# Performance work log

Measured on AMD Instinct MI355X. Metric: run time of the kernel, lower is better.

Reference implementation:

```python
import jax, jax.numpy as jnp
import numpy as np

PI = 3.14159265358979323846
MARGIN = 6.0
DIM = 256
ENT_TOT = 43234
REL_RANGE = (6.0 + 2.0) / DIM  # (margin + epsilon) / dim = 0.03125


def setup_inputs() -> dict:
    key = jax.random.key(0)
    k1, k2, k3 = jax.random.split(key, 3)
    head = jax.random.normal(k1, (32, 2 * DIM), dtype=jnp.float32)
    relation = jax.random.normal(k2, (32, DIM), dtype=jnp.float32)
    ent_emb = jax.random.normal(k3, (ENT_TOT, 2 * DIM), dtype=jnp.float32)
    return {"head": head, "relation": relation, "ent_emb": ent_emb}


def reference(head, relation, ent_emb):
    # head: (B, 2D) -> re/im halves (B, D)
    re_h, im_h = jnp.split(head, 2, axis=-1)
    # entity table: (E, 2D) -> (E, D) each
    re_t, im_t = jnp.split(ent_emb, 2, axis=-1)
    # phase rotation from relation embedding
    phase = relation / (REL_RANGE / PI)          # (B, D)
    re_r = jnp.cos(phase)
    im_r = jnp.sin(phase)
    # complex rotation of head by relation: (B, D)
    re_rot = re_h * re_r - im_h * im_r
    im_rot = re_h * im_r + im_h * re_r
    # difference against every entity, broadcast to (B, E, D)
    re_s = re_rot[:, None, :] - re_t[None, :, :]
    im_s = im_rot[:, None, :] - im_t[None, :, :]
    # L2 norm over the complex pair, summed over D -> (B, E)
    dist = jnp.sqrt(re_s * re_s + im_s * im_s).sum(axis=-1)
    return MARGIN - dist
```

## Files before the change

### kernel.cpp

```cpp
#include <hip/hip_runtime.h>
#include <math.h>

#define DIMH 256
#define NB   32
#define E_TOT 43234
#define TE   32
#define DK   64
#define PHASE_SCALE 100.53096491487338

__global__ void rot_kernel(const float* __restrict__ head,
                           const float* __restrict__ rel,
                           float* __restrict__ rot) {
    int b = blockIdx.x;
    int d = threadIdx.x;
    float re_h = head[b * 2 * DIMH + d];
    float im_h = head[b * 2 * DIMH + DIMH + d];
    float ph_f = rel[b * DIMH + d] * (float)PHASE_SCALE;
    double s, c;
    sincos((double)ph_f, &s, &c);
    float re_r = (float)c, im_r = (float)s;
    rot[b * DIMH + d]             = re_h * re_r - im_h * im_r;
    rot[NB * DIMH + b * DIMH + d] = re_h * im_r + im_h * re_r;
}

__device__ __forceinline__ float cplx_abs(float a, float b) {
    return __builtin_amdgcn_sqrtf(fmaf(a, a, b * b));
}

__global__ __launch_bounds__(256) void dist_kernel(const float* __restrict__ ent,
                                                   const float* __restrict__ rot,
                                                   float* __restrict__ out) {
    __shared__ float s_er[TE][DK + 2];
    __shared__ float s_ei[TE][DK + 2];
    __shared__ float s_rr[NB][DK + 2];
    __shared__ float s_ri[NB][DK + 2];

    const int tid = threadIdx.x;
    const int eb  = blockIdx.x * TE;
    const int e0  = (tid & 15) * 2;
    const int b0  = (tid >> 4) * 2;

    float acc00 = 0.f, acc01 = 0.f, acc10 = 0.f, acc11 = 0.f;

    for (int dk = 0; dk < DIMH; dk += DK) {
        #pragma unroll
        for (int qq = 0; qq < 2; ++qq) {
            int q   = tid + qq * 256;
            int row = q >> 4;
            int col = (q & 15) << 2;
            int er  = min(eb + row, E_TOT - 1);
            float4 vre = *reinterpret_cast<const float4*>(&ent[(size_t)er * (2 * DIMH) + dk + col]);
            float4 vim = *reinterpret_cast<const float4*>(&ent[(size_t)er * (2 * DIMH) + DIMH + dk + col]);
            float4 vrr = *reinterpret_cast<const float4*>(&rot[row * DIMH + dk + col]);
            float4 vri = *reinterpret_cast<const float4*>(&rot[NB * DIMH + row * DIMH + dk + col]);
            s_er[row][col + 0] = vre.x; s_er[row][col + 1] = vre.y; s_er[row][col + 2] = vre.z; s_er[row][col + 3] = vre.w;
            s_ei[row][col + 0] = vim.x; s_ei[row][col + 1] = vim.y; s_ei[row][col + 2] = vim.z; s_ei[row][col + 3] = vim.w;
            s_rr[row][col + 0] = vrr.x; s_rr[row][col + 1] = vrr.y; s_rr[row][col + 2] = vrr.z; s_rr[row][col + 3] = vrr.w;
            s_ri[row][col + 0] = vri.x; s_ri[row][col + 1] = vri.y; s_ri[row][col + 2] = vri.z; s_ri[row][col + 3] = vri.w;
        }
        __syncthreads();

        #pragma unroll
        for (int d = 0; d < DK; d += 2) {
            float2 rr0 = *reinterpret_cast<const float2*>(&s_rr[b0    ][d]);
            float2 rr1 = *reinterpret_cast<const float2*>(&s_rr[b0 + 1][d]);
            float2 ri0 = *reinterpret_cast<const float2*>(&s_ri[b0    ][d]);
            float2 ri1 = *reinterpret_cast<const float2*>(&s_ri[b0 + 1][d]);
            float2 er0 = *reinterpret_cast<const float2*>(&s_er[e0    ][d]);
            float2 er1 = *reinterpret_cast<const float2*>(&s_er[e0 + 1][d]);
            float2 ei0 = *reinterpret_cast<const float2*>(&s_ei[e0    ][d]);
            float2 ei1 = *reinterpret_cast<const float2*>(&s_ei[e0 + 1][d]);

            acc00 += cplx_abs(rr0.x - er0.x, ri0.x - ei0.x) + cplx_abs(rr0.y - er0.y, ri0.y - ei0.y);
            acc01 += cplx_abs(rr0.x - er1.x, ri0.x - ei1.x) + cplx_abs(rr0.y - er1.y, ri0.y - ei1.y);
            acc10 += cplx_abs(rr1.x - er0.x, ri1.x - ei0.x) + cplx_abs(rr1.y - er0.y, ri1.y - ei0.y);
            acc11 += cplx_abs(rr1.x - er1.x, ri1.x - ei1.x) + cplx_abs(rr1.y - er1.y, ri1.y - ei1.y);
        }
        __syncthreads();
    }

    const int e = eb + e0;
    if (e + 1 < E_TOT) {
        float2 o0 = make_float2(6.0f - acc00, 6.0f - acc01);
        float2 o1 = make_float2(6.0f - acc10, 6.0f - acc11);
        *reinterpret_cast<float2*>(&out[(size_t)b0 * E_TOT + e])       = o0;
        *reinterpret_cast<float2*>(&out[(size_t)(b0 + 1) * E_TOT + e]) = o1;
    } else if (e < E_TOT) {
        out[(size_t)b0 * E_TOT + e]       = 6.0f - acc00;
        out[(size_t)(b0 + 1) * E_TOT + e] = 6.0f - acc10;
    }
}

extern "C" void kernel_launch(void* const* d_in, const int* in_sizes, int n_in,
                              void* d_out, int out_size, void* d_ws, size_t ws_size,
                              hipStream_t stream) {
    const float* head = (const float*)d_in[0];
    const float* rel  = (const float*)d_in[1];
    const float* ent  = (const float*)d_in[2];
    float* rot = (float*)d_ws;

    rot_kernel<<<NB, DIMH, 0, stream>>>(head, rel, rot);

    int nblocks = (E_TOT + TE - 1) / TE;
    dist_kernel<<<nblocks, 256, 0, stream>>>(ent, rot, (float*)d_out);
}
```

Before: 202.2 us.

## Retile distance kernel to 64 entities per block with packed float2 math

Doubles the entity tile to 64 and halves the dimension chunk to 32. Each thread now computes 2 batches by 4 entities using packed two-wide vector arithmetic, so every rotated-head load is reused across more entities. The rotation kernel switches from double-precision sincos to single-precision sincosf, and shared-memory stores become float2 writes. Occupancy is hinted with a launch bound. The risks are more accumulator registers, a partially unrolled inner loop, and a small change in phase precision.

```diff
diff --git a/kernel.cpp b/kernel.cpp
--- a/kernel.cpp
+++ b/kernel.cpp
@@ -4,32 +4,38 @@
 #define DIMH 256
 #define NB   32
 #define E_TOT 43234
-#define TE   32
-#define DK   64
-#define PHASE_SCALE 100.53096491487338
+#define TE   64
+#define DK   32
+#define NCHUNK (DIMH / DK)
+#define PHASE_DIV 0.009947183943243459f
+
+typedef float v2f __attribute__((ext_vector_type(2)));
 
 __global__ void rot_kernel(const float* __restrict__ head,
                            const float* __restrict__ rel,
                            float* __restrict__ rot) {
-    int b = blockIdx.x;
-    int d = threadIdx.x;
+    int i = blockIdx.x * blockDim.x + threadIdx.x;
+    int b = i >> 8;
+    int d = i & 255;
     float re_h = head[b * 2 * DIMH + d];
     float im_h = head[b * 2 * DIMH + DIMH + d];
-    float ph_f = rel[b * DIMH + d] * (float)PHASE_SCALE;
-    double s, c;
-    sincos((double)ph_f, &s, &c);
-    float re_r = (float)c, im_r = (float)s;
-    rot[b * DIMH + d]             = re_h * re_r - im_h * im_r;
-    rot[NB * DIMH + b * DIMH + d] = re_h * im_r + im_h * re_r;
+    float ph = rel[b * DIMH + d] / PHASE_DIV;
+    float s, c;
+    sincosf(ph, &s, &c);
+    rot[b * DIMH + d]             = re_h * c - im_h * s;
+    rot[NB * DIMH + b * DIMH + d] = re_h * s + im_h * c;
 }
 
-__device__ __forceinline__ float cplx_abs(float a, float b) {
-    return __builtin_amdgcn_sqrtf(fmaf(a, a, b * b));
+__device__ __forceinline__ v2f sqrt2(v2f s) {
+    v2f r;
+    r.x = __builtin_amdgcn_sqrtf(s.x);
+    r.y = __builtin_amdgcn_sqrtf(s.y);
+    return r;
 }
 
-__global__ __launch_bounds__(256) void dist_kernel(const float* __restrict__ ent,
-                                                   const float* __restrict__ rot,
-                                                   float* __restrict__ out) {
+__global__ __launch_bounds__(256, 5) void dist_kernel(const float* __restrict__ ent,
+                                                      const float* __restrict__ rot,
+                                                      float* __restrict__ out) {
     __shared__ float s_er[TE][DK + 2];
     __shared__ float s_ei[TE][DK + 2];
     __shared__ float s_rr[NB][DK + 2];
@@ -37,57 +43,72 @@
 
     const int tid = threadIdx.x;
     const int eb  = blockIdx.x * TE;
-    const int e0  = (tid & 15) * 2;
+    const int g   = tid & 15;
     const int b0  = (tid >> 4) * 2;
 
-    float acc00 = 0.f, acc01 = 0.f, acc10 = 0.f, acc11 = 0.f;
+    v2f acc0[4], acc1[4];
+    #pragma unroll
+    for (int k = 0; k < 4; ++k) {
+        acc0[k].x = 0.f; acc0[k].y = 0.f;
+        acc1[k].x = 0.f; acc1[k].y = 0.f;
+    }
 
-    for (int dk = 0; dk < DIMH; dk += DK) {
+    for (int c = 0; c < NCHUNK; ++c) {
+        const int dk = c * DK;
         #pragma unroll
         for (int qq = 0; qq < 2; ++qq) {
             int q   = tid + qq * 256;
-            int row = q >> 4;
-            int col = (q & 15) << 2;
-            int er  = min(eb + row, E_TOT - 1);
+            int row = q >> 3;
+            int col = (q & 7) << 2;
+            int er  = eb + row;
+            if (er >= E_TOT) er = E_TOT - 1;
             float4 vre = *reinterpret_cast<const float4*>(&ent[(size_t)er * (2 * DIMH) + dk + col]);
             float4 vim = *reinterpret_cast<const float4*>(&ent[(size_t)er * (2 * DIMH) + DIMH + dk + col]);
+            *reinterpret_cast<float2*>(&s_er[row][col])     = make_float2(vre.x, vre.y);
+            *reinterpret_cast<float2*>(&s_er[row][col + 2]) = make_float2(vre.z, vre.w);
+            *reinterpret_cast<float2*>(&s_ei[row][col])     = make_float2(vim.x, vim.y);
+            *reinterpret_cast<float2*>(&s_ei[row][col + 2]) = make_float2(vim.z, vim.w);
+        }
+        {
+            int row = tid >> 3;
+            int col = (tid & 7) << 2;
             float4 vrr = *reinterpret_cast<const float4*>(&rot[row * DIMH + dk + col]);
             float4 vri = *reinterpret_cast<const float4*>(&rot[NB * DIMH + row * DIMH + dk + col]);
-            s_er[row][col + 0] = vre.x; s_er[row][col + 1] = vre.y; s_er[row][col + 2] = vre.z; s_er[row][col + 3] = vre.w;
-            s_ei[row][col + 0] = vim.x; s_ei[row][col + 1] = vim.y; s_ei[row][col + 2] = vim.z; s_ei[row][col + 3] = vim.w;
-            s_rr[row][col + 0] = vrr.x; s_rr[row][col + 1] = vrr.y; s_rr[row][col + 2] = vrr.z; s_rr[row][col + 3] = vrr.w;
-            s_ri[row][col + 0] = vri.x; s_ri[row][col + 1] = vri.y; s_ri[row][col + 2] = vri.z; s_ri[row][col + 3] = vri.w;
+            *reinterpret_cast<float2*>(&s_rr[row][col])     = make_float2(vrr.x, vrr.y);
+            *reinterpret_cast<float2*>(&s_rr[row][col + 2]) = make_float2(vrr.z, vrr.w);
+            *reinterpret_cast<float2*>(&s_ri[row][col])     = make_float2(vri.x, vri.y);
+            *reinterpret_cast<float2*>(&s_ri[row][col + 2]) = make_float2(vri.z, vri.w);
         }
         __syncthreads();
 
-        #pragma unroll
+        #pragma unroll 2
         for (int d = 0; d < DK; d += 2) {
-            float2 rr0 = *reinterpret_cast<const float2*>(&s_rr[b0    ][d]);
-            float2 rr1 = *reinterpret_cast<const float2*>(&s_rr[b0 + 1][d]);
-            float2 ri0 = *reinterpret_cast<const float2*>(&s_ri[b0    ][d]);
-            float2 ri1 = *reinterpret_cast<const float2*>(&s_ri[b0 + 1][d]);
-            float2 er0 = *reinterpret_cast<const float2*>(&s_er[e0    ][d]);
-            float2 er1 = *reinterpret_cast<const float2*>(&s_er[e0 + 1][d]);
-            float2 ei0 = *reinterpret_cast<const float2*>(&s_ei[e0    ][d]);
-            float2 ei1 = *reinterpret_cast<const float2*>(&s_ei[e0 + 1][d]);
-
-            acc00 += cplx_abs(rr0.x - er0.x, ri0.x - ei0.x) + cplx_abs(rr0.y - er0.y, ri0.y - ei0.y);
-            acc01 += cplx_abs(rr0.x - er1.x, ri0.x - ei1.x) + cplx_abs(rr0.y - er1.y, ri0.y - ei1.y);
-            acc10 += cplx_abs(rr1.x - er0.x, ri1.x - ei0.x) + cplx_abs(rr1.y - er0.y, ri1.y - ei0.y);
-            acc11 += cplx_abs(rr1.x - er1.x, ri1.x - ei1.x) + cplx_abs(rr1.y - er1.y, ri1.y - ei1.y);
+            v2f rr0 = *reinterpret_cast<const v2f*>(&s_rr[b0    ][d]);
+            v2f rr1 = *reinterpret_cast<const v2f*>(&s_rr[b0 + 1][d]);
+            v2f ri0 = *reinterpret_cast<const v2f*>(&s_ri[b0    ][d]);
+            v2f ri1 = *reinterpret_cast<const v2f*>(&s_ri[b0 + 1][d]);
+            #pragma unroll
+            for (int k = 0; k < 4; ++k) {
+                v2f er = *reinterpret_cast<const v2f*>(&s_er[g + 16 * k][d]);
+                v2f ei = *reinterpret_cast<const v2f*>(&s_ei[g + 16 * k][d]);
+                v2f a0 = rr0 - er, c0 = ri0 - ei;
+                v2f a1 = rr1 - er, c1 = ri1 - ei;
+                v2f s0 = a0 * a0 + c0 * c0;
+                v2f s1 = a1 * a1 + c1 * c1;
+                acc0[k] += sqrt2(s0);
+                acc1[k] += sqrt2(s1);
+            }
         }
         __syncthreads();
     }
 
-    const int e = eb + e0;
-    if (e + 1 < E_TOT) {
-        float2 o0 = make_float2(6.0f - acc00, 6.0f - acc01);
-        float2 o1 = make_float2(6.0f - acc10, 6.0f - acc11);
-        *reinterpret_cast<float2*>(&out[(size_t)b0 * E_TOT + e])       = o0;
-        *reinterpret_cast<float2*>(&out[(size_t)(b0 + 1) * E_TOT + e]) = o1;
-    } else if (e < E_TOT) {
-        out[(size_t)b0 * E_TOT + e]       = 6.0f - acc00;
-        out[(size_t)(b0 + 1) * E_TOT + e] = 6.0f - acc10;
+    #pragma unroll
+    for (int k = 0; k < 4; ++k) {
+        int e = eb + g + 16 * k;
+        if (e < E_TOT) {
+            out[(size_t)b0 * E_TOT + e]       = 6.0f - (acc0[k].x + acc0[k].y);
+            out[(size_t)(b0 + 1) * E_TOT + e] = 6.0f - (acc1[k].x + acc1[k].y);
+        }
     }
 }
 
@@ -99,7 +120,7 @@
     const float* ent  = (const float*)d_in[2];
     float* rot = (float*)d_ws;
 
-    rot_kernel<<<NB, DIMH, 0, stream>>>(head, rel, rot);
+    rot_kernel<<<(NB * DIMH) / 256, 256, 0, stream>>>(head, rel, rot);
 
     int nblocks = (E_TOT + TE - 1) / TE;
     dist_kernel<<<nblocks, 256, 0, stream>>>(ent, rot, (float*)d_out);
```

Result: faster. 179.8 us (-11.1%).
